# Performance work log

Measured on AMD Instinct MI355X. Metric: run time of the kernel, lower is better.

Reference implementation:

```python
import jax, jax.numpy as jnp
import numpy as np

BH, L, D = 64, 1024, 128

def setup_inputs() -> dict:
    key = jax.random.key(0)
    k1, k2, k3 = jax.random.split(key, 3)
    q = jax.random.normal(k1, (BH, L, D), dtype=jnp.float32)
    k = jax.random.normal(k2, (BH, L, D), dtype=jnp.float32)
    v = jax.random.normal(k3, (BH, L, D), dtype=jnp.float32)
    # causal multiplicative mask, broadcast to all batch*head slices
    attn_mask = jnp.broadcast_to(jnp.tril(jnp.ones((L, L), dtype=jnp.float32)), (BH, L, L))
    return {"q": q, "k": k, "v": v, "attn_mask": attn_mask}

def reference(q, k, v, attn_mask):
    # NOTE: original module computes self.temper = dim_dec**0.5 but never uses it,
    # so scores are UNscaled. Dropout is identity at eval.
    attn = jnp.einsum('bqd,bkd->bqk', q, k)          # [BH, L, L]
    attn = attn * attn_mask                           # multiplicative mask on logits
    attn = jnp.exp(attn - jnp.max(attn))              # GLOBAL max subtraction (not per-row)
    attn = attn * attn_mask                           # mask again after exp
    attn = attn / (jnp.sum(attn, axis=2, keepdims=True) + 1e-15)
    return jnp.einsum('bqk,bkd->bqd', attn, v)        # [BH, L, D]
```

## Files before the change

### kernel.cpp

```cpp
#include <hip/hip_runtime.h>
#include <hip/hip_bf16.h>

#define BHN 64
#define LSEQ 1024
#define DIM 128
#define BM 64
#define BN 64
#define NQB (LSEQ / BM)

typedef _Float16 f16x4 __attribute__((ext_vector_type(4)));
typedef _Float16 f16x8 __attribute__((ext_vector_type(8)));
typedef float f32x4 __attribute__((ext_vector_type(4)));

__global__ __launch_bounds__(256, 2) void attn_pass1(
    const float* __restrict__ Q, const float* __restrict__ K,
    const float* __restrict__ V, float* __restrict__ Out,
    float* __restrict__ mrow, float* __restrict__ rrow, float* __restrict__ gmax)
{
    __shared__ _Float16 Kf[2][BN][136];
    __shared__ _Float16 Vt[2][DIM][72];

    const int tid  = threadIdx.x;
    const int wave = tid >> 6;
    const int lane = tid & 63;
    const int g    = lane >> 4;
    const int ln   = lane & 15;
    const int bh   = blockIdx.x;
    const int p    = blockIdx.y;

    const float* qp = Q + (size_t)bh * LSEQ * DIM;
    const float* kp = K + (size_t)bh * LSEQ * DIM;
    const float* vp = V + (size_t)bh * LSEQ * DIM;

    const int vd = tid & 127;
    const int vh = tid >> 7;

    float4 kreg[8];
    float  vreg[4][8];

    auto issue = [&](int kv0) {
        #pragma unroll
        for (int i = 0; i < 8; ++i) {
            const int f4  = i * 256 + tid;
            const int row = f4 >> 5;
            const int c   = (f4 & 31) * 4;
            kreg[i] = *(const float4*)(kp + (size_t)(kv0 + row) * DIM + c);
        }
        #pragma unroll
        for (int nb = 0; nb < 4; ++nb)
            #pragma unroll
            for (int i = 0; i < 8; ++i)
                vreg[nb][i] = vp[(size_t)(kv0 + vh * 32 + nb * 8 + i) * DIM + vd];
    };

    int cur = 0;
    issue(0);

    for (int s = 0; s < 2; ++s) {
        const int qb    = s ? (NQB - 1 - p) : p;
        const int qrow0 = qb * BM + wave * 16;

        f16x8 qf[4];
        {
            const float* qrow = qp + (size_t)(qrow0 + ln) * DIM;
            #pragma unroll
            for (int kc = 0; kc < 4; ++kc) {
                const int d0 = kc * 32 + g * 8;
                float4 f0 = *(const float4*)(qrow + d0);
                float4 f1 = *(const float4*)(qrow + d0 + 4);
                f16x8 h;
                h[0] = (_Float16)f0.x; h[1] = (_Float16)f0.y;
                h[2] = (_Float16)f0.z; h[3] = (_Float16)f0.w;
                h[4] = (_Float16)f1.x; h[5] = (_Float16)f1.y;
                h[6] = (_Float16)f1.z; h[7] = (_Float16)f1.w;
                qf[kc] = h;
            }
        }

        float m_st = -1e30f, r_st = 0.f;
        f32x4 o_acc[8];
        #pragma unroll
        for (int d = 0; d < 8; ++d) { f32x4 z = {0.f,0.f,0.f,0.f}; o_acc[d] = z; }

        const int nt = qb + 1;
        for (int t = 0; t < nt; ++t) {
            const int kv0 = t * BN;

            f16x4 khf[8];
            #pragma unroll
            for (int i = 0; i < 8; ++i) {
                f16x4 h4;
                h4[0] = (_Float16)kreg[i].x; h4[1] = (_Float16)kreg[i].y;
                h4[2] = (_Float16)kreg[i].z; h4[3] = (_Float16)kreg[i].w;
                khf[i] = h4;
            }
            f16x8 vbf[4];
            #pragma unroll
            for (int nb = 0; nb < 4; ++nb) {
                f16x8 w;
                #pragma unroll
                for (int i = 0; i < 8; ++i) w[i] = (_Float16)vreg[nb][i];
                vbf[nb] = w;
            }

            __syncthreads();
            #pragma unroll
            for (int i = 0; i < 8; ++i) {
                const int f4  = i * 256 + tid;
                const int row = f4 >> 5;
                const int c   = (f4 & 31) * 4;
                *(f16x4*)&Kf[cur][row][c] = khf[i];
            }
            #pragma unroll
            for (int nb = 0; nb < 4; ++nb)
                *(f16x8*)&Vt[cur][vd][vh * 32 + nb * 8] = vbf[nb];
            __syncthreads();

            const int nxt = (t + 1 < nt) ? (t + 1) * BN : (s == 0 ? 0 : -1);
            if (nxt >= 0) issue(nxt);

            f32x4 sacc[4];
            #pragma unroll
            for (int ns = 0; ns < 4; ++ns) { f32x4 z = {0.f,0.f,0.f,0.f}; sacc[ns] = z; }
            #pragma unroll
            for (int ns = 0; ns < 4; ++ns) {
                const int n = ns * 16 + ln;
                #pragma unroll
                for (int kc = 0; kc < 4; ++kc) {
                    f16x8 kh_ = *(const f16x8*)&Kf[cur][n][kc * 32 + g * 8];
                    sacc[ns] = __builtin_amdgcn_mfma_f32_16x16x32_f16(kh_, qf[kc], sacc[ns], 0, 0, 0);
                }
            }

            if (t == qb) {
                const int qm = qrow0 + ln - kv0 - 4 * g;
                #pragma unroll
                for (int ns = 0; ns < 4; ++ns)
                    #pragma unroll
                    for (int j = 0; j < 4; ++j)
                        if (16 * ns + j > qm) sacc[ns][j] = -1e30f;
            }

            float tm = -1e30f;
            #pragma unroll
            for (int ns = 0; ns < 4; ++ns)
                #pragma unroll
                for (int j = 0; j < 4; ++j) tm = fmaxf(tm, sacc[ns][j]);
            tm = fmaxf(tm, __shfl_xor(tm, 16));
            tm = fmaxf(tm, __shfl_xor(tm, 32));
            const float mn = fmaxf(m_st, tm);
            const float sc = __expf(m_st - mn);
            float pr[4][4];
            float ts = 0.f;
            #pragma unroll
            for (int ns = 0; ns < 4; ++ns)
                #pragma unroll
                for (int j = 0; j < 4; ++j) {
                    const float pv = __expf(sacc[ns][j] - mn);
                    pr[ns][j] = pv;
                    ts += pv;
                }
            ts += __shfl_xor(ts, 16);
            ts += __shfl_xor(ts, 32);
            r_st = r_st * sc + ts;
            m_st = mn;

            float scr[4];
            #pragma unroll
            for (int r = 0; r < 4; ++r) scr[r] = __shfl(sc, 4 * g + r);
            #pragma unroll
            for (int d = 0; d < 8; ++d) {
                o_acc[d][0] *= scr[0]; o_acc[d][1] *= scr[1];
                o_acc[d][2] *= scr[2]; o_acc[d][3] *= scr[3];
            }

            f16x8 pa0, pa1;
            #pragma unroll
            for (int j = 0; j < 4; ++j) {
                pa0[j]     = (_Float16)pr[0][j];
                pa0[4 + j] = (_Float16)pr[1][j];
                pa1[j]     = (_Float16)pr[2][j];
                pa1[4 + j] = (_Float16)pr[3][j];
            }
            #pragma unroll
            for (int ds = 0; ds < 8; ++ds) {
                const int dc = ds * 16 + ln;
                f16x4 v0 = *(const f16x4*)&Vt[cur][dc][4 * g];
                f16x4 v1 = *(const f16x4*)&Vt[cur][dc][16 + 4 * g];
                f16x8 bv0;
                #pragma unroll
                for (int j = 0; j < 4; ++j) { bv0[j] = v0[j]; bv0[4 + j] = v1[j]; }
                o_acc[ds] = __builtin_amdgcn_mfma_f32_16x16x32_f16(pa0, bv0, o_acc[ds], 0, 0, 0);
                f16x4 v2 = *(const f16x4*)&Vt[cur][dc][32 + 4 * g];
                f16x4 v3 = *(const f16x4*)&Vt[cur][dc][48 + 4 * g];
                f16x8 bv1;
                #pragma unroll
                for (int j = 0; j < 4; ++j) { bv1[j] = v2[j]; bv1[4 + j] = v3[j]; }
                o_acc[ds] = __builtin_amdgcn_mfma_f32_16x16x32_f16(pa1, bv1, o_acc[ds], 0, 0, 0);
            }

            cur ^= 1;
        }

        #pragma unroll
        for (int ds = 0; ds < 8; ++ds) {
            const int dc = ds * 16 + ln;
            #pragma unroll
            for (int r = 0; r < 4; ++r) {
                const int qr = qrow0 + g * 4 + r;
                Out[((size_t)bh * LSEQ + qr) * DIM + dc] = o_acc[ds][r];
            }
        }
        if (lane < 16) {
            mrow[bh * LSEQ + qrow0 + lane] = m_st;
            rrow[bh * LSEQ + qrow0 + lane] = r_st;
        }
        float bm = m_st;
        #pragma unroll
        for (int off = 32; off >= 1; off >>= 1) bm = fmaxf(bm, __shfl_xor(bm, off));
        if (lane == 0) atomicMax((int*)gmax, __float_as_int(bm));
    }
}

__global__ __launch_bounds__(256) void attn_epilogue(
    float* __restrict__ Out, const float* __restrict__ mrow,
    const float* __restrict__ rrow, const float* __restrict__ gmax)
{
    const int idx = blockIdx.x * 256 + threadIdx.x;
    const int row = idx >> 5;
    const float M = *gmax;
    float e = M - mrow[row] - 34.538776394910684f;
    e = fminf(e, 85.f);
    const float denom = rrow[row] + __expf(e);
    const float inv = 1.0f / denom;
    float4 o = ((float4*)Out)[idx];
    o.x *= inv; o.y *= inv; o.z *= inv; o.w *= inv;
    ((float4*)Out)[idx] = o;
}

extern "C" void kernel_launch(void* const* d_in, const int* in_sizes, int n_in,
                              void* d_out, int out_size, void* d_ws, size_t ws_size,
                              hipStream_t stream)
{
    const float* q = (const float*)d_in[0];
    const float* k = (const float*)d_in[1];
    const float* v = (const float*)d_in[2];
    float* out  = (float*)d_out;
    float* mrow = (float*)d_ws;
    float* rrow = mrow + BHN * LSEQ;
    float* gmax = rrow + BHN * LSEQ;

    hipMemsetAsync(gmax, 0, sizeof(float), stream);

    dim3 grid(BHN, NQB / 2);
    attn_pass1<<<grid, 256, 0, stream>>>(q, k, v, out, mrow, rrow, gmax);

    const int n4 = BHN * LSEQ * DIM / 4;
    attn_epilogue<<<n4 / 256, 256, 0, stream>>>(out, mrow, rrow, gmax);
}
```

Measured before the change: 96.07 us.

## Use 128-row query tiles with 8 waves and heaviest-first block scheduling

Query tiles grow to 128 rows per block with 512 threads (8 waves), so each K/V tile staged in shared memory is shared by twice as many query rows. The paired light/heavy query-block loop is replaced by a flat 1D grid that launches the largest causal blocks first. The pipeline is restructured so the fp16 conversion and store of the next tile overlap with compute, using one barrier per iteration; waves whose rows lie entirely above the current tile skip it. LDS padding shrinks and the occupancy hint rises. The costs are causal load imbalance between waves in the same block and more register pressure under the tighter launch bounds.

```diff
diff --git a/kernel.cpp b/kernel.cpp
--- a/kernel.cpp
+++ b/kernel.cpp
@@ -4,7 +4,7 @@
 #define BHN 64
 #define LSEQ 1024
 #define DIM 128
-#define BM 64
+#define BM 128
 #define BN 64
 #define NQB (LSEQ / BM)
 
@@ -12,21 +12,24 @@
 typedef _Float16 f16x8 __attribute__((ext_vector_type(8)));
 typedef float f32x4 __attribute__((ext_vector_type(4)));
 
-__global__ __launch_bounds__(256, 2) void attn_pass1(
+__global__ __launch_bounds__(512, 4) void attn_pass1(
     const float* __restrict__ Q, const float* __restrict__ K,
     const float* __restrict__ V, float* __restrict__ Out,
     float* __restrict__ mrow, float* __restrict__ rrow, float* __restrict__ gmax)
 {
-    __shared__ _Float16 Kf[2][BN][136];
-    __shared__ _Float16 Vt[2][DIM][72];
+    __shared__ _Float16 Kf[2][BN][132];
+    __shared__ _Float16 Vt[2][DIM][68];
 
     const int tid  = threadIdx.x;
     const int wave = tid >> 6;
     const int lane = tid & 63;
     const int g    = lane >> 4;
     const int ln   = lane & 15;
-    const int bh   = blockIdx.x;
-    const int p    = blockIdx.y;
+    const int L    = blockIdx.x;
+    const int i6   = (L >> 6) & 7;
+    const int qb   = (L < 256) ? (NQB - 1 - i6) : (i6 & 3);
+    const int bh   = L & 63;
+    const int qrow0 = qb * BM + wave * 16;
 
     const float* qp = Q + (size_t)bh * LSEQ * DIM;
     const float* kp = K + (size_t)bh * LSEQ * DIM;
@@ -35,90 +38,83 @@
     const int vd = tid & 127;
     const int vh = tid >> 7;
 
-    float4 kreg[8];
-    float  vreg[4][8];
+    float4 kreg[4];
+    float  vreg[2][8];
 
     auto issue = [&](int kv0) {
         #pragma unroll
-        for (int i = 0; i < 8; ++i) {
-            const int f4  = i * 256 + tid;
+        for (int i = 0; i < 4; ++i) {
+            const int f4  = i * 512 + tid;
             const int row = f4 >> 5;
             const int c   = (f4 & 31) * 4;
             kreg[i] = *(const float4*)(kp + (size_t)(kv0 + row) * DIM + c);
         }
         #pragma unroll
-        for (int nb = 0; nb < 4; ++nb)
+        for (int nb = 0; nb < 2; ++nb)
             #pragma unroll
             for (int i = 0; i < 8; ++i)
-                vreg[nb][i] = vp[(size_t)(kv0 + vh * 32 + nb * 8 + i) * DIM + vd];
+                vreg[nb][i] = vp[(size_t)(kv0 + vh * 16 + nb * 8 + i) * DIM + vd];
     };
 
+    auto convert_stage = [&](int b) {
+        #pragma unroll
+        for (int i = 0; i < 4; ++i) {
+            const int f4  = i * 512 + tid;
+            const int row = f4 >> 5;
+            const int c   = (f4 & 31) * 4;
+            f16x4 h4;
+            h4[0] = (_Float16)kreg[i].x; h4[1] = (_Float16)kreg[i].y;
+            h4[2] = (_Float16)kreg[i].z; h4[3] = (_Float16)kreg[i].w;
+            *(f16x4*)&Kf[b][row][c] = h4;
+        }
+        #pragma unroll
+        for (int nb = 0; nb < 2; ++nb) {
+            f16x8 w;
+            #pragma unroll
+            for (int i = 0; i < 8; ++i) w[i] = (_Float16)vreg[nb][i];
+            *(f16x8*)&Vt[b][vd][vh * 16 + nb * 8] = w;
+        }
+    };
+
+    f16x8 qf[4];
+    {
+        const float* qrow = qp + (size_t)(qrow0 + ln) * DIM;
+        #pragma unroll
+        for (int kc = 0; kc < 4; ++kc) {
+            const int d0 = kc * 32 + g * 8;
+            float4 f0 = *(const float4*)(qrow + d0);
+            float4 f1 = *(const float4*)(qrow + d0 + 4);
+            f16x8 h;
+            h[0] = (_Float16)f0.x; h[1] = (_Float16)f0.y;
+            h[2] = (_Float16)f0.z; h[3] = (_Float16)f0.w;
+            h[4] = (_Float16)f1.x; h[5] = (_Float16)f1.y;
+            h[6] = (_Float16)f1.z; h[7] = (_Float16)f1.w;
+            qf[kc] = h;
+        }
+    }
+
+    float m_st = -1e30f, r_st = 0.f;
+    f32x4 o_acc[8];
+    #pragma unroll
+    for (int d = 0; d < 8; ++d) { f32x4 z = {0.f,0.f,0.f,0.f}; o_acc[d] = z; }
+
+    const int nt = 2 * qb + 2;
+
+    issue(0);
+    convert_stage(0);
+    if (nt > 1) issue(BN);
+    __syncthreads();
+
     int cur = 0;
-    issue(0);
-
-    for (int s = 0; s < 2; ++s) {
-        const int qb    = s ? (NQB - 1 - p) : p;
-        const int qrow0 = qb * BM + wave * 16;
-
-        f16x8 qf[4];
-        {
-            const float* qrow = qp + (size_t)(qrow0 + ln) * DIM;
-            #pragma unroll
-            for (int kc = 0; kc < 4; ++kc) {
-                const int d0 = kc * 32 + g * 8;
-                float4 f0 = *(const float4*)(qrow + d0);
-                float4 f1 = *(const float4*)(qrow + d0 + 4);
-                f16x8 h;
-                h[0] = (_Float16)f0.x; h[1] = (_Float16)f0.y;
-                h[2] = (_Float16)f0.z; h[3] = (_Float16)f0.w;
-                h[4] = (_Float16)f1.x; h[5] = (_Float16)f1.y;
-                h[6] = (_Float16)f1.z; h[7] = (_Float16)f1.w;
-                qf[kc] = h;
-            }
-        }
-
-        float m_st = -1e30f, r_st = 0.f;
-        f32x4 o_acc[8];
-        #pragma unroll
-        for (int d = 0; d < 8; ++d) { f32x4 z = {0.f,0.f,0.f,0.f}; o_acc[d] = z; }
-
-        const int nt = qb + 1;
-        for (int t = 0; t < nt; ++t) {
-            const int kv0 = t * BN;
-
-            f16x4 khf[8];
-            #pragma unroll
-            for (int i = 0; i < 8; ++i) {
-                f16x4 h4;
-                h4[0] = (_Float16)kreg[i].x; h4[1] = (_Float16)kreg[i].y;
-                h4[2] = (_Float16)kreg[i].z; h4[3] = (_Float16)kreg[i].w;
-                khf[i] = h4;
-            }
-            f16x8 vbf[4];
-            #pragma unroll
-            for (int nb = 0; nb < 4; ++nb) {
-                f16x8 w;
-                #pragma unroll
-                for (int i = 0; i < 8; ++i) w[i] = (_Float16)vreg[nb][i];
-                vbf[nb] = w;
-            }
-
-            __syncthreads();
-            #pragma unroll
-            for (int i = 0; i < 8; ++i) {
-                const int f4  = i * 256 + tid;
-                const int row = f4 >> 5;
-                const int c   = (f4 & 31) * 4;
-                *(f16x4*)&Kf[cur][row][c] = khf[i];
-            }
-            #pragma unroll
-            for (int nb = 0; nb < 4; ++nb)
-                *(f16x8*)&Vt[cur][vd][vh * 32 + nb * 8] = vbf[nb];
-            __syncthreads();
-
-            const int nxt = (t + 1 < nt) ? (t + 1) * BN : (s == 0 ? 0 : -1);
-            if (nxt >= 0) issue(nxt);
-
+    for (int t = 0; t < nt; ++t) {
+        const int kv0 = t * BN;
+
+        if (t + 1 < nt) {
+            convert_stage(cur ^ 1);
+            if (t + 2 < nt) issue((t + 2) * BN);
+        }
+
+        if (qrow0 + 15 >= kv0) {
             f32x4 sacc[4];
             #pragma unroll
             for (int ns = 0; ns < 4; ++ns) { f32x4 z = {0.f,0.f,0.f,0.f}; sacc[ns] = z; }
@@ -132,7 +128,7 @@
                 }
             }
 
-            if (t == qb) {
+            if (kv0 + BN - 1 > qrow0) {
                 const int qm = qrow0 + ln - kv0 - 4 * g;
                 #pragma unroll
                 for (int ns = 0; ns < 4; ++ns)
@@ -198,28 +194,29 @@
                 for (int j = 0; j < 4; ++j) { bv1[j] = v2[j]; bv1[4 + j] = v3[j]; }
                 o_acc[ds] = __builtin_amdgcn_mfma_f32_16x16x32_f16(pa1, bv1, o_acc[ds], 0, 0, 0);
             }
-
-            cur ^= 1;
-        }
-
-        #pragma unroll
-        for (int ds = 0; ds < 8; ++ds) {
-            const int dc = ds * 16 + ln;
-            #pragma unroll
-            for (int r = 0; r < 4; ++r) {
-                const int qr = qrow0 + g * 4 + r;
-                Out[((size_t)bh * LSEQ + qr) * DIM + dc] = o_acc[ds][r];
-            }
-        }
-        if (lane < 16) {
-            mrow[bh * LSEQ + qrow0 + lane] = m_st;
-            rrow[bh * LSEQ + qrow0 + lane] = r_st;
-        }
-        float bm = m_st;
-        #pragma unroll
-        for (int off = 32; off >= 1; off >>= 1) bm = fmaxf(bm, __shfl_xor(bm, off));
-        if (lane == 0) atomicMax((int*)gmax, __float_as_int(bm));
-    }
+        }
+
+        __syncthreads();
+        cur ^= 1;
+    }
+
+    #pragma unroll
+    for (int ds = 0; ds < 8; ++ds) {
+        const int dc = ds * 16 + ln;
+        #pragma unroll
+        for (int r = 0; r < 4; ++r) {
+            const int qr = qrow0 + g * 4 + r;
+            Out[((size_t)bh * LSEQ + qr) * DIM + dc] = o_acc[ds][r];
+        }
+    }
+    if (lane < 16) {
+        mrow[bh * LSEQ + qrow0 + lane] = m_st;
+        rrow[bh * LSEQ + qrow0 + lane] = r_st;
+    }
+    float bm = m_st;
+    #pragma unroll
+    for (int off = 32; off >= 1; off >>= 1) bm = fmaxf(bm, __shfl_xor(bm, off));
+    if (lane == 0) atomicMax((int*)gmax, __float_as_int(bm));
 }
 
 __global__ __launch_bounds__(256) void attn_epilogue(
@@ -252,8 +249,7 @@
 
     hipMemsetAsync(gmax, 0, sizeof(float), stream);
 
-    dim3 grid(BHN, NQB / 2);
-    attn_pass1<<<grid, 256, 0, stream>>>(q, k, v, out, mrow, rrow, gmax);
+    attn_pass1<<<dim3(BHN * NQB), 512, 0, stream>>>(q, k, v, out, mrow, rrow, gmax);
 
     const int n4 = BHN * LSEQ * DIM / 4;
     attn_epilogue<<<n4 / 256, 256, 0, stream>>>(out, mrow, rrow, gmax);
```

Measured after the change: 91.91 us. -4.3%, faster.
